# Performance work log

Hardware: AMD Instinct MI355X
Metric: run time of the kernel (lower is better)

## Reference

```python
import jax, jax.numpy as jnp
import numpy as np

D_MODEL = 1024
NUM_HEADS = 16
DEPTH = D_MODEL // NUM_HEADS
MAX_SEQ = 2048
B, S = 2, 2048


def setup_inputs() -> dict:
    key = jax.random.key(0)
    ks = jax.random.split(key, 12)
    scale = 1.0 / np.sqrt(D_MODEL)
    inp = {
        'q': jax.random.normal(ks[0], (B, S, D_MODEL), jnp.float32),
        'k': jax.random.normal(ks[1], (B, S, D_MODEL), jnp.float32),
        'v': jax.random.normal(ks[2], (B, S, D_MODEL), jnp.float32),
        'mask': jnp.zeros((B, 1, S, S), jnp.float32),
        'wq_w': jax.random.normal(ks[3], (D_MODEL, D_MODEL), jnp.float32) * scale,
        'wq_b': jnp.zeros((D_MODEL,), jnp.float32),
        'wk_w': jax.random.normal(ks[4], (D_MODEL, D_MODEL), jnp.float32) * scale,
        'wk_b': jnp.zeros((D_MODEL,), jnp.float32),
        'wv_w': jax.random.normal(ks[5], (D_MODEL, D_MODEL), jnp.float32) * scale,
        'wv_b': jnp.zeros((D_MODEL,), jnp.float32),
        'dense_w': jax.random.normal(ks[6], (D_MODEL, D_MODEL), jnp.float32) * scale,
        'dense_b': jnp.zeros((D_MODEL,), jnp.float32),
        'rel_bias': jax.random.normal(ks[7], (2 * MAX_SEQ - 1, NUM_HEADS), jnp.float32),
    }
    return inp


def _split_heads(x):
    # [B, S, D_MODEL] -> [B, H, S, depth]
    b, s, _ = x.shape
    return x.reshape(b, s, NUM_HEADS, DEPTH).transpose(0, 2, 1, 3)


def reference(q, k, v, mask, wq_w, wq_b, wk_w, wk_b, wv_w, wv_b, dense_w, dense_b, rel_bias):
    b, s, _ = q.shape
    # torch Linear: y = x @ W.T + b
    qh = _split_heads(q @ wq_w.T + wq_b)
    kh = _split_heads(k @ wk_w.T + wk_b)
    vh = _split_heads(v @ wv_w.T + wv_b)
    logits = jnp.einsum('bhqd,bhkd->bhqk', qh, kh) / jnp.sqrt(jnp.float32(DEPTH))
    # relative position bias gather
    pos = jnp.arange(s)
    idx = jnp.clip(pos[:, None] - pos[None, :] + MAX_SEQ - 1, 0, 2 * MAX_SEQ - 2)  # [S, S]
    pos_bias = rel_bias[idx]                      # [S, S, H]
    pos_bias = pos_bias.transpose(2, 0, 1)[None]  # [1, H, S, S]
    logits = logits + pos_bias + mask * (-1e9)
    attn = jax.nn.softmax(logits, axis=-1)        # dropout is identity in eval
    out = jnp.einsum('bhqk,bhkd->bhqd', attn, vh)
    out = out.transpose(0, 2, 1, 3).reshape(b, s, D_MODEL)
    out = out @ dense_w.T + dense_b
    return out, attn
```

## Files before the change

kernel.cpp:

```cpp
#include <hip/hip_runtime.h>

typedef _Float16 f16x8 __attribute__((ext_vector_type(8)));
typedef _Float16 f16x4 __attribute__((ext_vector_type(4)));
typedef float f32x4 __attribute__((ext_vector_type(4)));
typedef unsigned short u16x8 __attribute__((ext_vector_type(8)));
typedef unsigned int u32;

#define MFMA16H(a, b, c) __builtin_amdgcn_mfma_f32_16x16x32_f16(a, b, c, 0, 0, 0)

#if __has_builtin(__builtin_amdgcn_exp2f)
#define EXP2F(x) __builtin_amdgcn_exp2f(x)
#else
#define EXP2F(x) exp2f(x)
#endif

#define LOG2E 1.44269504088896340736f
#define SHIFT2 14.0f

__device__ __forceinline__ unsigned short f2bf(float x) {
  unsigned u = __float_as_uint(x);
  u += 0x7FFF + ((u >> 16) & 1);
  return (unsigned short)(u >> 16);
}
__device__ __forceinline__ float bf2f(unsigned short h) {
  return __uint_as_float(((unsigned)h) << 16);
}
__device__ __forceinline__ f16x8 ldh8(const _Float16* p) {
  return *reinterpret_cast<const f16x8*>(p);
}
__device__ __forceinline__ u16x8 ldu8(const unsigned short* p) {
  return *reinterpret_cast<const u16x8*>(p);
}
__device__ __forceinline__ void gload_lds16(const void* g, void* lds) {
  __builtin_amdgcn_global_load_lds(
      (const __attribute__((address_space(1))) u32*)g,
      (__attribute__((address_space(3))) u32*)lds, 16, 0, 0);
}

__global__ __launch_bounds__(256) void prep_f16(const float* __restrict__ src,
                                                _Float16* __restrict__ dst, int n4) {
  int i = blockIdx.x * 256 + threadIdx.x;
  if (i >= n4) return;
  float4 x = reinterpret_cast<const float4*>(src)[i];
  f16x4 h;
  h[0] = (_Float16)x.x; h[1] = (_Float16)x.y;
  h[2] = (_Float16)x.z; h[3] = (_Float16)x.w;
  reinterpret_cast<f16x4*>(dst)[i] = h;
}

__global__ __launch_bounds__(256) void prep_mask_perm(const float* __restrict__ src,
                                                      unsigned short* __restrict__ dst) {
  const int blk = blockIdx.x;
  const int kt = blk & 31, bq = blk >> 5;
  const int b = bq >> 5, qt = bq & 31;
  const int lane = threadIdx.x;
  const int w = lane >> 6, lg = (lane >> 4) & 3, lr = lane & 15;
  const int q0 = qt * 64;
  const float cs = -1e9f * LOG2E;
  unsigned short vals[16];
#pragma unroll
  for (int c = 0; c < 4; ++c)
#pragma unroll
    for (int r = 0; r < 4; ++r) {
      const int qr = q0 + w * 16 + lg * 4 + r;
      const int kc = kt * 64 + c * 16 + lr;
      vals[c * 4 + r] = f2bf(src[((size_t)b * 2048 + qr) * 2048 + kc] * cs);
    }
  uint4* out = reinterpret_cast<uint4*>(dst) + ((size_t)blk * 256 + lane) * 2;
  out[0] = *reinterpret_cast<uint4*>(&vals[0]);
  out[1] = *reinterpret_cast<uint4*>(&vals[8]);
}

template <int MODE>
__global__ __launch_bounds__(256) void gemm_kernel(
    const _Float16* __restrict__ A, const _Float16* __restrict__ B,
    const float* __restrict__ bias,
    _Float16* __restrict__ out_h, float* __restrict__ out_f) {
  __shared__ __align__(16) _Float16 As[128 * 32];
  __shared__ __align__(16) _Float16 Bs[128 * 32];

  const int tid = threadIdx.x;
  const int tm = blockIdx.x & 31, tn = blockIdx.x >> 5;
  const int m0 = tm * 128, n0 = tn * 128;
  const int w = tid >> 6, l = tid & 63, lg = l >> 4, lr = l & 15;
  const int wr = w >> 1, wc = w & 1;
  const int srow = tid >> 2, scol = (tid & 3) * 8;

  f32x4 acc[4][4] = {};

  for (int kt = 0; kt < 32; ++kt) {
    const int k0 = kt * 32;
    uint4 ra[2], rb[2];
#pragma unroll
    for (int it = 0; it < 2; ++it) {
      const int row = it * 64 + srow;
      ra[it] = *reinterpret_cast<const uint4*>(A + (size_t)(m0 + row) * 1024 + k0 + scol);
      rb[it] = *reinterpret_cast<const uint4*>(B + (size_t)(n0 + row) * 1024 + k0 + scol);
    }
    __syncthreads();
#pragma unroll
    for (int it = 0; it < 2; ++it) {
      const int eo = (it * 256 + tid) * 8;
      *reinterpret_cast<uint4*>(As + eo) = ra[it];
      *reinterpret_cast<uint4*>(Bs + eo) = rb[it];
    }
    __syncthreads();

    f16x8 fa[4], fb[4];
#pragma unroll
    for (int i = 0; i < 4; ++i) {
      fa[i] = ldh8(As + (wr * 64 + i * 16 + lr) * 32 + lg * 8);
      fb[i] = ldh8(Bs + (wc * 64 + i * 16 + lr) * 32 + lg * 8);
    }
#pragma unroll
    for (int i = 0; i < 4; ++i)
#pragma unroll
      for (int j = 0; j < 4; ++j)
        acc[i][j] = MFMA16H(fa[i], fb[j], acc[i][j]);
    __syncthreads();
  }

#pragma unroll
  for (int i = 0; i < 4; ++i) {
    const int mrow = m0 + wr * 64 + i * 16 + lg * 4;
#pragma unroll
    for (int j = 0; j < 4; ++j) {
      const int ncol = n0 + wc * 64 + j * 16 + lr;
      const float bv = bias[ncol];
#pragma unroll
      for (int r = 0; r < 4; ++r) {
        const int m = mrow + r;
        const float v = acc[i][j][r] + bv;
        if (MODE == 2) {
          out_f[(size_t)m * 1024 + ncol] = v;
        } else {
          const int bb = m >> 11, s = m & 2047, hh = ncol >> 6, d = ncol & 63;
          if (MODE == 0)
            out_h[((size_t)(bb * 16 + hh) * 2048 + s) * 64 + d] = (_Float16)v;
          else
            out_h[((size_t)(bb * 16 + hh) * 64 + d) * 2048 + s] = (_Float16)v;
        }
      }
    }
  }
}

__global__ __launch_bounds__(256) void attn_pv_kernel(
    const _Float16* __restrict__ qh, const _Float16* __restrict__ kh,
    const _Float16* __restrict__ vT,
    const float* __restrict__ rel_bias, const unsigned short* __restrict__ mperm,
    _Float16* __restrict__ o_h, float* __restrict__ scal) {
  __shared__ float rb2[2112];
  __shared__ __align__(16) _Float16 khs[64 * 64];
  __shared__ __align__(16) _Float16 p_lds[64 * 76];

  const int bid = blockIdx.x;
  const int wg = ((bid & 7) << 7) | (bid >> 3);
  const int bh = wg >> 5, qt = wg & 31;
  const int b = bh >> 4, h = bh & 15;
  const int q0 = qt * 64;
  const int tid = threadIdx.x;
  const int w = tid >> 6, l = tid & 63, lg = l >> 4, lr = l & 15;

  for (int t = tid; t < 2112; t += 256)
    rb2[t] = rel_bias[(q0 + t) * 16 + h] * LOG2E - SHIFT2;

  const size_t bh_off = (size_t)bh * 2048 * 64;
  const _Float16* qhb = qh + bh_off;
  const char* khb = (const char*)(kh + bh_off);
  const _Float16* vTb = vT + bh_off;
  const unsigned short* mpb =
      mperm + (((size_t)(b * 32 + qt) * 32) * 256 + tid) * 16;

  f16x8 qf[2];
  {
    const size_t qrow = (size_t)(q0 + w * 16 + lr) * 64;
    qf[0] = ldh8(qhb + qrow + lg * 8);
    qf[1] = ldh8(qhb + qrow + 32 + lg * 8);
  }

  const int qbase = w * 16 + lg * 4;
  const float c1 = 0.125f * LOG2E;
  float sacc[4] = {0.f, 0.f, 0.f, 0.f};
  f32x4 acc_o[4] = {};
  const int e0 = w * 2 * 64 + l;

  for (int kt = 0; kt < 32; ++kt) {
    __syncthreads();
#pragma unroll
    for (int cc = 0; cc < 2; ++cc) {
      const int e = e0 + cc * 64;
      const int row = e >> 3, colb = (e & 7) << 4;
      const int srcb = (row << 7) + (colb ^ ((row & 7) << 4));
      gload_lds16(khb + (size_t)kt * 8192 + srcb, (char*)khs + e * 16);
    }
    u16x8 m0v = ldu8(mpb + (size_t)kt * 256 * 16);
    u16x8 m1v = ldu8(mpb + (size_t)kt * 256 * 16 + 8);
    f16x8 vf[4][2];
#pragma unroll
    for (int n = 0; n < 4; ++n)
#pragma unroll
      for (int j = 0; j < 2; ++j)
        vf[n][j] = ldh8(vTb + (size_t)(n * 16 + lr) * 2048 + kt * 64 + j * 32 + lg * 8);
    __syncthreads();

#pragma unroll
    for (int c = 0; c < 4; ++c) {
      const int rowk = c * 16 + lr;
      f32x4 acc = {};
#pragma unroll
      for (int kk = 0; kk < 2; ++kk) {
        const int off = (rowk << 7) + (((kk << 6) + (lg << 4)) ^ ((rowk & 7) << 4));
        acc = MFMA16H(qf[kk], ldh8((const _Float16*)((const char*)khs + off)), acc);
      }
      const int kc = kt * 64 + c * 16 + lr;
#pragma unroll
      for (int r = 0; r < 4; ++r) {
        const float mbf = bf2f((c < 2) ? (unsigned short)m0v[(c & 1) * 4 + r]
                                       : (unsigned short)m1v[(c & 1) * 4 + r]);
        const float l2 = fmaf(acc[r], c1, rb2[qbase + r - kc + 2047]) + mbf;
        const float p = EXP2F(l2);
        sacc[r] += p;
        p_lds[(qbase + r) * 76 + c * 16 + lr] = (_Float16)p;
      }
    }

    f16x8 pf0 = ldh8(p_lds + (w * 16 + lr) * 76 + lg * 8);
    f16x8 pf1 = ldh8(p_lds + (w * 16 + lr) * 76 + 32 + lg * 8);
#pragma unroll
    for (int n = 0; n < 4; ++n) {
      acc_o[n] = MFMA16H(pf0, vf[n][0], acc_o[n]);
      acc_o[n] = MFMA16H(pf1, vf[n][1], acc_o[n]);
    }
  }

  float inv_s[4];
#pragma unroll
  for (int r = 0; r < 4; ++r) {
    float s = sacc[r];
    s += __shfl_xor(s, 1);
    s += __shfl_xor(s, 2);
    s += __shfl_xor(s, 4);
    s += __shfl_xor(s, 8);
    inv_s[r] = 1.0f / s;
    if (lr == 0) scal[(size_t)bh * 2048 + q0 + qbase + r] = inv_s[r];
  }

#pragma unroll
  for (int n = 0; n < 4; ++n)
#pragma unroll
    for (int r = 0; r < 4; ++r) {
      const int qr = q0 + qbase + r;
      const int d = n * 16 + lr;
      o_h[((size_t)(b * 2048 + qr) * 16 + h) * 64 + d] = (_Float16)(acc_o[n][r] * inv_s[r]);
    }
}

__global__ __launch_bounds__(256) void attn_write_kernel(
    const _Float16* __restrict__ qh, const _Float16* __restrict__ kh,
    const float* __restrict__ rel_bias, const unsigned short* __restrict__ mperm,
    const float* __restrict__ scal, float* __restrict__ attn_out) {
  __shared__ float rb2[2112];
  __shared__ __align__(16) _Float16 khs[64 * 64];
  __shared__ __align__(16) float p32[64 * 68];

  const int bid = blockIdx.x;
  const int wg = ((bid & 7) << 7) | (bid >> 3);
  const int bh = wg >> 5, qt = wg & 31;
  const int b = bh >> 4, h = bh & 15;
  const int q0 = qt * 64;
  const int tid = threadIdx.x;
  const int w = tid >> 6, l = tid & 63, lg = l >> 4, lr = l & 15;

  for (int t = tid; t < 2112; t += 256)
    rb2[t] = rel_bias[(q0 + t) * 16 + h] * LOG2E - SHIFT2;

  const size_t bh_off = (size_t)bh * 2048 * 64;
  const _Float16* qhb = qh + bh_off;
  const char* khb = (const char*)(kh + bh_off);
  const unsigned short* mpb =
      mperm + (((size_t)(b * 32 + qt) * 32) * 256 + tid) * 16;
  float* attn_bh = attn_out + (size_t)bh * 2048 * 2048;

  f16x8 qf[2];
  {
    const size_t qrow = (size_t)(q0 + w * 16 + lr) * 64;
    qf[0] = ldh8(qhb + qrow + lg * 8);
    qf[1] = ldh8(qhb + qrow + 32 + lg * 8);
  }

  const int qbase = w * 16 + lg * 4;
  const float c1 = 0.125f * LOG2E;
  float4 inv4 = *reinterpret_cast<const float4*>(scal + (size_t)bh * 2048 + q0 + qbase);
  const float invs[4] = {inv4.x, inv4.y, inv4.z, inv4.w};

  const int srow = w * 16 + (l >> 2);
  const int scb = (l & 3) * 16;
  const int e0 = w * 2 * 64 + l;

  for (int kt = 0; kt < 32; ++kt) {
    __syncthreads();
#pragma unroll
    for (int cc = 0; cc < 2; ++cc) {
      const int e = e0 + cc * 64;
      const int row = e >> 3, colb = (e & 7) << 4;
      const int srcb = (row << 7) + (colb ^ ((row & 7) << 4));
      gload_lds16(khb + (size_t)kt * 8192 + srcb, (char*)khs + e * 16);
    }
    u16x8 m0v = ldu8(mpb + (size_t)kt * 256 * 16);
    u16x8 m1v = ldu8(mpb + (size_t)kt * 256 * 16 + 8);
    __syncthreads();

#pragma unroll
    for (int c = 0; c < 4; ++c) {
      const int rowk = c * 16 + lr;
      f32x4 acc = {};
#pragma unroll
      for (int kk = 0; kk < 2; ++kk) {
        const int off = (rowk << 7) + (((kk << 6) + (lg << 4)) ^ ((rowk & 7) << 4));
        acc = MFMA16H(qf[kk], ldh8((const _Float16*)((const char*)khs + off)), acc);
      }
      const int kc = kt * 64 + c * 16 + lr;
#pragma unroll
      for (int r = 0; r < 4; ++r) {
        const float mbf = bf2f((c < 2) ? (unsigned short)m0v[(c & 1) * 4 + r]
                                       : (unsigned short)m1v[(c & 1) * 4 + r]);
        const float l2 = fmaf(acc[r], c1, rb2[qbase + r - kc + 2047]) + mbf;
        p32[(qbase + r) * 68 + c * 16 + lr] = EXP2F(l2) * invs[r];
      }
    }

    float* arow = attn_bh + (size_t)(q0 + srow) * 2048 + kt * 64 + scb;
#pragma unroll
    for (int i = 0; i < 4; ++i)
      *reinterpret_cast<float4*>(arow + i * 4) =
          *reinterpret_cast<const float4*>(&p32[srow * 68 + scb + i * 4]);
  }
}

extern "C" void kernel_launch(void* const* d_in, const int* in_sizes, int n_in,
                              void* d_out, int out_size, void* d_ws, size_t ws_size,
                              hipStream_t stream) {
  const float* q = (const float*)d_in[0];
  const float* k = (const float*)d_in[1];
  const float* v = (const float*)d_in[2];
  const float* mask = (const float*)d_in[3];
  const float* wq_w = (const float*)d_in[4];
  const float* wq_b = (const float*)d_in[5];
  const float* wk_w = (const float*)d_in[6];
  const float* wk_b = (const float*)d_in[7];
  const float* wv_w = (const float*)d_in[8];
  const float* wv_b = (const float*)d_in[9];
  const float* dw = (const float*)d_in[10];
  const float* db = (const float*)d_in[11];
  const float* rel = (const float*)d_in[12];

  char* ws = (char*)d_ws;
  _Float16* qf   = (_Float16*)(ws + 0);
  _Float16* kf   = (_Float16*)(ws + 8388608);
  _Float16* vf   = (_Float16*)(ws + 16777216);
  _Float16* wqf  = (_Float16*)(ws + 25165824);
  _Float16* wkf  = (_Float16*)(ws + 27262976);
  _Float16* wvf  = (_Float16*)(ws + 29360128);
  _Float16* dwf  = (_Float16*)(ws + 31457280);
  _Float16* qhf  = (_Float16*)(ws + 33554432);
  _Float16* khf  = (_Float16*)(ws + 41943040);
  _Float16* vhT  = (_Float16*)(ws + 50331648);
  _Float16* o_h  = (_Float16*)(ws + 58720256);
  float* scal    = (float*)(ws + 67108864);
  unsigned short* mperm = (unsigned short*)(ws + 67371008);

  float* out = (float*)d_out;
  float* attn_out = out + 4194304;

  prep_f16<<<4096, 256, 0, stream>>>(q, qf, 1048576);
  prep_f16<<<4096, 256, 0, stream>>>(k, kf, 1048576);
  prep_f16<<<4096, 256, 0, stream>>>(v, vf, 1048576);
  prep_f16<<<1024, 256, 0, stream>>>(wq_w, wqf, 262144);
  prep_f16<<<1024, 256, 0, stream>>>(wk_w, wkf, 262144);
  prep_f16<<<1024, 256, 0, stream>>>(wv_w, wvf, 262144);
  prep_f16<<<1024, 256, 0, stream>>>(dw, dwf, 262144);
  prep_mask_perm<<<2048, 256, 0, stream>>>(mask, mperm);

  gemm_kernel<0><<<256, 256, 0, stream>>>(qf, wqf, wq_b, qhf, nullptr);
  gemm_kernel<0><<<256, 256, 0, stream>>>(kf, wkf, wk_b, khf, nullptr);
  gemm_kernel<1><<<256, 256, 0, stream>>>(vf, wvf, wv_b, vhT, nullptr);

  attn_pv_kernel<<<1024, 256, 0, stream>>>(qhf, khf, vhT, rel, mperm, o_h, scal);
  attn_write_kernel<<<1024, 256, 0, stream>>>(qhf, khf, rel, mperm, scal, attn_out);

  gemm_kernel<2><<<256, 256, 0, stream>>>(o_h, dwf, db, nullptr, out);
}
```

Measured before the change: 651.0 us.

## Fuse fp32-to-f16 conversion into GEMMs and read K directly from global

Removes the seven standalone fp32-to-f16 prep kernels. The conversion now happens inside the GEMM tile loads, and the Q/K/V projections run as a single 768-block launch. The attention kernels drop LDS staging of K and the per-tile barriers, loading K and V fragments straight from global memory, and add occupancy hints via launch bounds. The GEMMs also drop the redundant trailing barrier. The trade-off is that the GEMMs now read fp32 operands at twice the bytes, and attention relies on cache hits instead of shared K reuse across waves.

Result: faster. 606.7 us (-6.8%).

```diff
diff --git a/kernel.cpp b/kernel.cpp
--- a/kernel.cpp
+++ b/kernel.cpp
@@ -31,21 +31,11 @@
 __device__ __forceinline__ u16x8 ldu8(const unsigned short* p) {
   return *reinterpret_cast<const u16x8*>(p);
 }
-__device__ __forceinline__ void gload_lds16(const void* g, void* lds) {
-  __builtin_amdgcn_global_load_lds(
-      (const __attribute__((address_space(1))) u32*)g,
-      (__attribute__((address_space(3))) u32*)lds, 16, 0, 0);
-}
-
-__global__ __launch_bounds__(256) void prep_f16(const float* __restrict__ src,
-                                                _Float16* __restrict__ dst, int n4) {
-  int i = blockIdx.x * 256 + threadIdx.x;
-  if (i >= n4) return;
-  float4 x = reinterpret_cast<const float4*>(src)[i];
-  f16x4 h;
-  h[0] = (_Float16)x.x; h[1] = (_Float16)x.y;
-  h[2] = (_Float16)x.z; h[3] = (_Float16)x.w;
-  reinterpret_cast<f16x4*>(dst)[i] = h;
+__device__ __forceinline__ f16x8 cvt8(float4 a, float4 b) {
+  f16x8 r;
+  r[0] = (_Float16)a.x; r[1] = (_Float16)a.y; r[2] = (_Float16)a.z; r[3] = (_Float16)a.w;
+  r[4] = (_Float16)b.x; r[5] = (_Float16)b.y; r[6] = (_Float16)b.z; r[7] = (_Float16)b.w;
+  return r;
 }
 
 __global__ __launch_bounds__(256) void prep_mask_perm(const float* __restrict__ src,
@@ -71,11 +61,89 @@
   out[1] = *reinterpret_cast<uint4*>(&vals[8]);
 }
 
-template <int MODE>
-__global__ __launch_bounds__(256) void gemm_kernel(
-    const _Float16* __restrict__ A, const _Float16* __restrict__ B,
-    const float* __restrict__ bias,
-    _Float16* __restrict__ out_h, float* __restrict__ out_f) {
+__global__ __launch_bounds__(256, 3) void proj_gemm_kernel(
+    const float* __restrict__ qin, const float* __restrict__ kin, const float* __restrict__ vin,
+    const float* __restrict__ wq, const float* __restrict__ wk, const float* __restrict__ wv,
+    const float* __restrict__ bq, const float* __restrict__ bk, const float* __restrict__ bv,
+    _Float16* __restrict__ qhf, _Float16* __restrict__ khf, _Float16* __restrict__ vhT) {
+  __shared__ __align__(16) _Float16 As[128 * 32];
+  __shared__ __align__(16) _Float16 Bs[128 * 32];
+
+  const int mode = blockIdx.x >> 8;
+  const int t = blockIdx.x & 255;
+  const float* A = mode == 0 ? qin : (mode == 1 ? kin : vin);
+  const float* B = mode == 0 ? wq : (mode == 1 ? wk : wv);
+  const float* bias = mode == 0 ? bq : (mode == 1 ? bk : bv);
+  _Float16* outp = mode == 0 ? qhf : (mode == 1 ? khf : vhT);
+
+  const int tid = threadIdx.x;
+  const int tm = t & 31, tn = t >> 5;
+  const int m0 = tm * 128, n0 = tn * 128;
+  const int w = tid >> 6, l = tid & 63, lg = l >> 4, lr = l & 15;
+  const int wr = w >> 1, wc = w & 1;
+  const int srow = tid >> 2, scol = (tid & 3) * 8;
+
+  f32x4 acc[4][4] = {};
+
+  for (int kt = 0; kt < 32; ++kt) {
+    const int k0 = kt * 32;
+    float4 ra[2][2], rb[2][2];
+#pragma unroll
+    for (int it = 0; it < 2; ++it) {
+      const int row = it * 64 + srow;
+      const float* pa = A + (size_t)(m0 + row) * 1024 + k0 + scol;
+      const float* pb = B + (size_t)(n0 + row) * 1024 + k0 + scol;
+      ra[it][0] = *reinterpret_cast<const float4*>(pa);
+      ra[it][1] = *reinterpret_cast<const float4*>(pa + 4);
+      rb[it][0] = *reinterpret_cast<const float4*>(pb);
+      rb[it][1] = *reinterpret_cast<const float4*>(pb + 4);
+    }
+    __syncthreads();
+#pragma unroll
+    for (int it = 0; it < 2; ++it) {
+      const int eo = (it * 256 + tid) * 8;
+      *reinterpret_cast<f16x8*>(As + eo) = cvt8(ra[it][0], ra[it][1]);
+      *reinterpret_cast<f16x8*>(Bs + eo) = cvt8(rb[it][0], rb[it][1]);
+    }
+    __syncthreads();
+
+    f16x8 fa[4], fb[4];
+#pragma unroll
+    for (int i = 0; i < 4; ++i) {
+      fa[i] = ldh8(As + (wr * 64 + i * 16 + lr) * 32 + lg * 8);
+      fb[i] = ldh8(Bs + (wc * 64 + i * 16 + lr) * 32 + lg * 8);
+    }
+#pragma unroll
+    for (int i = 0; i < 4; ++i)
+#pragma unroll
+      for (int j = 0; j < 4; ++j)
+        acc[i][j] = MFMA16H(fa[i], fb[j], acc[i][j]);
+  }
+
+#pragma unroll
+  for (int i = 0; i < 4; ++i) {
+    const int mrow = m0 + wr * 64 + i * 16 + lg * 4;
+#pragma unroll
+    for (int j = 0; j < 4; ++j) {
+      const int ncol = n0 + wc * 64 + j * 16 + lr;
+      const float bv = bias[ncol];
+#pragma unroll
+      for (int r = 0; r < 4; ++r) {
+        const int m = mrow + r;
+        const float v = acc[i][j][r] + bv;
+        const int bb = m >> 11, s = m & 2047, hh = ncol >> 6, d = ncol & 63;
+        if (mode != 2)
+          outp[((size_t)(bb * 16 + hh) * 2048 + s) * 64 + d] = (_Float16)v;
+        else
+          outp[((size_t)(bb * 16 + hh) * 64 + d) * 2048 + s] = (_Float16)v;
+      }
+    }
+  }
+}
+
+__global__ __launch_bounds__(256) void dense_gemm_kernel(
+    const _Float16* __restrict__ A, const float* __restrict__ B,
+    const float* __restrict__ bias, float* __restrict__ out_f) {
   __shared__ __align__(16) _Float16 As[128 * 32];
   __shared__ __align__(16) _Float16 Bs[128 * 32];
 
@@ -90,19 +158,22 @@
 
   for (int kt = 0; kt < 32; ++kt) {
     const int k0 = kt * 32;
-    uint4 ra[2], rb[2];
+    uint4 ra[2];
+    float4 rb[2][2];
 #pragma unroll
     for (int it = 0; it < 2; ++it) {
       const int row = it * 64 + srow;
       ra[it] = *reinterpret_cast<const uint4*>(A + (size_t)(m0 + row) * 1024 + k0 + scol);
-      rb[it] = *reinterpret_cast<const uint4*>(B + (size_t)(n0 + row) * 1024 + k0 + scol);
+      const float* pb = B + (size_t)(n0 + row) * 1024 + k0 + scol;
+      rb[it][0] = *reinterpret_cast<const float4*>(pb);
+      rb[it][1] = *reinterpret_cast<const float4*>(pb + 4);
     }
     __syncthreads();
 #pragma unroll
     for (int it = 0; it < 2; ++it) {
       const int eo = (it * 256 + tid) * 8;
       *reinterpret_cast<uint4*>(As + eo) = ra[it];
-      *reinterpret_cast<uint4*>(Bs + eo) = rb[it];
+      *reinterpret_cast<f16x8*>(Bs + eo) = cvt8(rb[it][0], rb[it][1]);
     }
     __syncthreads();
 
@@ -117,7 +188,6 @@
 #pragma unroll
       for (int j = 0; j < 4; ++j)
         acc[i][j] = MFMA16H(fa[i], fb[j], acc[i][j]);
-    __syncthreads();
   }
 
 #pragma unroll
@@ -128,30 +198,18 @@
       const int ncol = n0 + wc * 64 + j * 16 + lr;
       const float bv = bias[ncol];
 #pragma unroll
-      for (int r = 0; r < 4; ++r) {
-        const int m = mrow + r;
-        const float v = acc[i][j][r] + bv;
-        if (MODE == 2) {
-          out_f[(size_t)m * 1024 + ncol] = v;
-        } else {
-          const int bb = m >> 11, s = m & 2047, hh = ncol >> 6, d = ncol & 63;
-          if (MODE == 0)
-            out_h[((size_t)(bb * 16 + hh) * 2048 + s) * 64 + d] = (_Float16)v;
-          else
-            out_h[((size_t)(bb * 16 + hh) * 64 + d) * 2048 + s] = (_Float16)v;
-        }
-      }
-    }
-  }
-}
-
-__global__ __launch_bounds__(256) void attn_pv_kernel(
+      for (int r = 0; r < 4; ++r)
+        out_f[(size_t)(mrow + r) * 1024 + ncol] = acc[i][j][r] + bv;
+    }
+  }
+}
+
+__global__ __launch_bounds__(256, 3) void attn_pv_kernel(
     const _Float16* __restrict__ qh, const _Float16* __restrict__ kh,
     const _Float16* __restrict__ vT,
     const float* __restrict__ rel_bias, const unsigned short* __restrict__ mperm,
     _Float16* __restrict__ o_h, float* __restrict__ scal) {
   __shared__ float rb2[2112];
-  __shared__ __align__(16) _Float16 khs[64 * 64];
   __shared__ __align__(16) _Float16 p_lds[64 * 76];
 
   const int bid = blockIdx.x;
@@ -162,12 +220,12 @@
   const int tid = threadIdx.x;
   const int w = tid >> 6, l = tid & 63, lg = l >> 4, lr = l & 15;
 
-  for (int t = tid; t < 2112; t += 256)
+  for (int t = tid; t < 2111; t += 256)
     rb2[t] = rel_bias[(q0 + t) * 16 + h] * LOG2E - SHIFT2;
 
   const size_t bh_off = (size_t)bh * 2048 * 64;
   const _Float16* qhb = qh + bh_off;
-  const char* khb = (const char*)(kh + bh_off);
+  const _Float16* khb = kh + bh_off;
   const _Float16* vTb = vT + bh_off;
   const unsigned short* mpb =
       mperm + (((size_t)(b * 32 + qt) * 32) * 256 + tid) * 16;
@@ -178,42 +236,23 @@
     qf[0] = ldh8(qhb + qrow + lg * 8);
     qf[1] = ldh8(qhb + qrow + 32 + lg * 8);
   }
+  __syncthreads();
 
   const int qbase = w * 16 + lg * 4;
   const float c1 = 0.125f * LOG2E;
   float sacc[4] = {0.f, 0.f, 0.f, 0.f};
   f32x4 acc_o[4] = {};
-  const int e0 = w * 2 * 64 + l;
 
   for (int kt = 0; kt < 32; ++kt) {
-    __syncthreads();
-#pragma unroll
-    for (int cc = 0; cc < 2; ++cc) {
-      const int e = e0 + cc * 64;
-      const int row = e >> 3, colb = (e & 7) << 4;
-      const int srcb = (row << 7) + (colb ^ ((row & 7) << 4));
-      gload_lds16(khb + (size_t)kt * 8192 + srcb, (char*)khs + e * 16);
-    }
-    u16x8 m0v = ldu8(mpb + (size_t)kt * 256 * 16);
-    u16x8 m1v = ldu8(mpb + (size_t)kt * 256 * 16 + 8);
-    f16x8 vf[4][2];
-#pragma unroll
-    for (int n = 0; n < 4; ++n)
-#pragma unroll
-      for (int j = 0; j < 2; ++j)
-        vf[n][j] = ldh8(vTb + (size_t)(n * 16 + lr) * 2048 + kt * 64 + j * 32 + lg * 8);
-    __syncthreads();
-
+    u16x8 m0v = ldu8(mpb + (size_t)kt * 4096);
+    u16x8 m1v = ldu8(mpb + (size_t)kt * 4096 + 8);
 #pragma unroll
     for (int c = 0; c < 4; ++c) {
-      const int rowk = c * 16 + lr;
+      const int kc = kt * 64 + c * 16 + lr;
+      const _Float16* kr = khb + (size_t)kc * 64 + lg * 8;
       f32x4 acc = {};
-#pragma unroll
-      for (int kk = 0; kk < 2; ++kk) {
-        const int off = (rowk << 7) + (((kk << 6) + (lg << 4)) ^ ((rowk & 7) << 4));
-        acc = MFMA16H(qf[kk], ldh8((const _Float16*)((const char*)khs + off)), acc);
-      }
-      const int kc = kt * 64 + c * 16 + lr;
+      acc = MFMA16H(qf[0], ldh8(kr), acc);
+      acc = MFMA16H(qf[1], ldh8(kr + 32), acc);
 #pragma unroll
       for (int r = 0; r < 4; ++r) {
         const float mbf = bf2f((c < 2) ? (unsigned short)m0v[(c & 1) * 4 + r]
@@ -224,13 +263,13 @@
         p_lds[(qbase + r) * 76 + c * 16 + lr] = (_Float16)p;
       }
     }
-
     f16x8 pf0 = ldh8(p_lds + (w * 16 + lr) * 76 + lg * 8);
     f16x8 pf1 = ldh8(p_lds + (w * 16 + lr) * 76 + 32 + lg * 8);
 #pragma unroll
     for (int n = 0; n < 4; ++n) {
-      acc_o[n] = MFMA16H(pf0, vf[n][0], acc_o[n]);
-      acc_o[n] = MFMA16H(pf1, vf[n][1], acc_o[n]);
+      const _Float16* vr = vTb + (size_t)(n * 16 + lr) * 2048 + kt * 64 + lg * 8;
+      acc_o[n] = MFMA16H(pf0, ldh8(vr), acc_o[n]);
+      acc_o[n] = MFMA16H(pf1, ldh8(vr + 32), acc_o[n]);
     }
   }
 
@@ -256,12 +295,11 @@
     }
 }
 
-__global__ __launch_bounds__(256) void attn_write_kernel(
+__global__ __launch_bounds__(256, 4) void attn_write_kernel(
     const _Float16* __restrict__ qh, const _Float16* __restrict__ kh,
     const float* __restrict__ rel_bias, const unsigned short* __restrict__ mperm,
     const float* __restrict__ scal, float* __restrict__ attn_out) {
   __shared__ float rb2[2112];
-  __shared__ __align__(16) _Float16 khs[64 * 64];
   __shared__ __align__(16) float p32[64 * 68];
 
   const int bid = blockIdx.x;
@@ -272,12 +310,12 @@
   const int tid = threadIdx.x;
   const int w = tid >> 6, l = tid & 63, lg = l >> 4, lr = l & 15;
 
-  for (int t = tid; t < 2112; t += 256)
+  for (int t = tid; t < 2111; t += 256)
     rb2[t] = rel_bias[(q0 + t) * 16 + h] * LOG2E - SHIFT2;
 
   const size_t bh_off = (size_t)bh * 2048 * 64;
   const _Float16* qhb = qh + bh_off;
-  const char* khb = (const char*)(kh + bh_off);
+  const _Float16* khb = kh + bh_off;
   const unsigned short* mpb =
       mperm + (((size_t)(b * 32 + qt) * 32) * 256 + tid) * 16;
   float* attn_bh = attn_out + (size_t)bh * 2048 * 2048;
@@ -288,6 +326,7 @@
     qf[0] = ldh8(qhb + qrow + lg * 8);
     qf[1] = ldh8(qhb + qrow + 32 + lg * 8);
   }
+  __syncthreads();
 
   const int qbase = w * 16 + lg * 4;
   const float c1 = 0.125f * LOG2E;
@@ -296,31 +335,17 @@
 
   const int srow = w * 16 + (l >> 2);
   const int scb = (l & 3) * 16;
-  const int e0 = w * 2 * 64 + l;
 
   for (int kt = 0; kt < 32; ++kt) {
-    __syncthreads();
-#pragma unroll
-    for (int cc = 0; cc < 2; ++cc) {
-      const int e = e0 + cc * 64;
-      const int row = e >> 3, colb = (e & 7) << 4;
-      const int srcb = (row << 7) + (colb ^ ((row & 7) << 4));
-      gload_lds16(khb + (size_t)kt * 8192 + srcb, (char*)khs + e * 16);
-    }
-    u16x8 m0v = ldu8(mpb + (size_t)kt * 256 * 16);
-    u16x8 m1v = ldu8(mpb + (size_t)kt * 256 * 16 + 8);
-    __syncthreads();
-
+    u16x8 m0v = ldu8(mpb + (size_t)kt * 4096);
+    u16x8 m1v = ldu8(mpb + (size_t)kt * 4096 + 8);
 #pragma unroll
     for (int c = 0; c < 4; ++c) {
-      const int rowk = c * 16 + lr;
+      const int kc = kt * 64 + c * 16 + lr;
+      const _Float16* kr = khb + (size_t)kc * 64 + lg * 8;
       f32x4 acc = {};
-#pragma unroll
-      for (int kk = 0; kk < 2; ++kk) {
-        const int off = (rowk << 7) + (((kk << 6) + (lg << 4)) ^ ((rowk & 7) << 4));
-        acc = MFMA16H(qf[kk], ldh8((const _Float16*)((const char*)khs + off)), acc);
-      }
-      const int kc = kt * 64 + c * 16 + lr;
+      acc = MFMA16H(qf[0], ldh8(kr), acc);
+      acc = MFMA16H(qf[1], ldh8(kr + 32), acc);
 #pragma unroll
       for (int r = 0; r < 4; ++r) {
         const float mbf = bf2f((c < 2) ? (unsigned short)m0v[(c & 1) * 4 + r]
@@ -329,7 +354,6 @@
         p32[(qbase + r) * 68 + c * 16 + lr] = EXP2F(l2) * invs[r];
       }
     }
-
     float* arow = attn_bh + (size_t)(q0 + srow) * 2048 + kt * 64 + scb;
 #pragma unroll
     for (int i = 0; i < 4; ++i)
@@ -356,38 +380,23 @@
   const float* rel = (const float*)d_in[12];
 
   char* ws = (char*)d_ws;
-  _Float16* qf   = (_Float16*)(ws + 0);
-  _Float16* kf   = (_Float16*)(ws + 8388608);
-  _Float16* vf   = (_Float16*)(ws + 16777216);
-  _Float16* wqf  = (_Float16*)(ws + 25165824);
-  _Float16* wkf  = (_Float16*)(ws + 27262976);
-  _Float16* wvf  = (_Float16*)(ws + 29360128);
-  _Float16* dwf  = (_Float16*)(ws + 31457280);
-  _Float16* qhf  = (_Float16*)(ws + 33554432);
-  _Float16* khf  = (_Float16*)(ws + 41943040);
-  _Float16* vhT  = (_Float16*)(ws + 50331648);
-  _Float16* o_h  = (_Float16*)(ws + 58720256);
-  float* scal    = (float*)(ws + 67108864);
-  unsigned short* mperm = (unsigned short*)(ws + 67371008);
+  _Float16* qhf  = (_Float16*)(ws + 0);
+  _Float16* khf  = (_Float16*)(ws + 8388608);
+  _Float16* vhT  = (_Float16*)(ws + 16777216);
+  _Float16* o_h  = (_Float16*)(ws + 25165824);
+  float* scal    = (float*)(ws + 33554432);
+  unsigned short* mperm = (unsigned short*)(ws + 33816576);
 
   float* out = (float*)d_out;
   float* attn_out = out + 4194304;
 
-  prep_f16<<<4096, 256, 0, stream>>>(q, qf, 1048576);
-  prep_f16<<<4096, 256, 0, stream>>>(k, kf, 1048576);
-  prep_f16<<<4096, 256, 0, stream>>>(v, vf, 1048576);
-  prep_f16<<<1024, 256, 0, stream>>>(wq_w, wqf, 262144);
-  prep_f16<<<1024, 256, 0, stream>>>(wk_w, wkf, 262144);
-  prep_f16<<<1024, 256, 0, stream>>>(wv_w, wvf, 262144);
-  prep_f16<<<1024, 256, 0, stream>>>(dw, dwf, 262144);
   prep_mask_perm<<<2048, 256, 0, stream>>>(mask, mperm);
 
-  gemm_kernel<0><<<256, 256, 0, stream>>>(qf, wqf, wq_b, qhf, nullptr);
-  gemm_kernel<0><<<256, 256, 0, stream>>>(kf, wkf, wk_b, khf, nullptr);
-  gemm_kernel<1><<<256, 256, 0, stream>>>(vf, wvf, wv_b, vhT, nullptr);
+  proj_gemm_kernel<<<768, 256, 0, stream>>>(q, k, v, wq_w, wk_w, wv_w,
+                                            wq_b, wk_b, wv_b, qhf, khf, vhT);
 
   attn_pv_kernel<<<1024, 256, 0, stream>>>(qhf, khf, vhT, rel, mperm, o_h, scal);
   attn_write_kernel<<<1024, 256, 0, stream>>>(qhf, khf, rel, mperm, scal, attn_out);
 
-  gemm_kernel<2><<<256, 256, 0, stream>>>(o_h, dwf, db, nullptr, out);
-}
+  dense_gemm_kernel<<<256, 256, 0, stream>>>(o_h, dw, db, out);
+}
```
